# Kernel optimization log

Hardware: AMD Instinct MI355X
Metric: run time of the kernel (lower is better)

Reference implementation:

```python
import jax, jax.numpy as jnp
import numpy as np

B, S, H, IN, OUT = 1024, 512, 512, 2, 2


def setup_inputs() -> dict:
    key = jax.random.key(0)
    ks = jax.random.split(key, 10)
    s = 1.0 / np.sqrt(H)  # torch default uniform init scale for GRU/Linear
    u = lambda k, shp: jax.random.uniform(k, shp, jnp.float32, -s, s)
    return {
        "X0": jax.random.normal(ks[0], (B, OUT), jnp.float32),
        "V": jax.random.normal(ks[1], (B, S, IN), jnp.float32),
        "W_ih": u(ks[2], (3 * H, IN + OUT)),
        "W_hh": u(ks[3], (3 * H, H)),
        "b_ih": u(ks[4], (3 * H,)),
        "b_hh": u(ks[5], (3 * H,)),
        "W1": u(ks[6], (H // 2, H)),
        "b1": u(ks[7], (H // 2,)),
        "W2": u(ks[8], (OUT, H // 2)),
        "b2": u(ks[9], (OUT,)),
    }


def reference(X0, V, W_ih, W_hh, b_ih, b_hh, W1, b1, W2, b2):
    out_size = W2.shape[0]
    hidden = W_hh.shape[1]

    def step(carry, v_t):
        x_prev, h_prev = carry  # [B,out], [B,H]
        linear_pred = x_prev + v_t[:, :out_size]
        gru_in = jnp.concatenate([v_t, x_prev], axis=-1)  # [B, in+out]
        gi = gru_in @ W_ih.T + b_ih  # [B, 3H]
        gh = h_prev @ W_hh.T + b_hh  # [B, 3H]
        i_r, i_z, i_n = jnp.split(gi, 3, axis=-1)
        h_r, h_z, h_n = jnp.split(gh, 3, axis=-1)
        r = jax.nn.sigmoid(i_r + h_r)
        z = jax.nn.sigmoid(i_z + h_z)
        n = jnp.tanh(i_n + r * h_n)
        h_t = (1.0 - z) * n + z * h_prev  # torch GRU cell update
        residual = jax.nn.relu(h_t @ W1.T + b1) @ W2.T + b2
        x_t = linear_pred + residual
        return (x_t, h_t), x_t

    h0 = jnp.zeros((X0.shape[0], hidden), X0.dtype)
    _, xs = jax.lax.scan(step, (X0, h0), jnp.swapaxes(V, 0, 1))  # xs: [S,B,out]
    return jnp.swapaxes(xs, 0, 1)  # [B,S,out]
```

## Files before the change

### kernel.cpp

```cpp
#include <hip/hip_runtime.h>

#define Ssz 512
#define BT  64
#define SLC 32

typedef __attribute__((ext_vector_type(8))) short short8;
typedef __attribute__((ext_vector_type(4))) float f32x4;
typedef __attribute__((ext_vector_type(4))) unsigned uint4v;

#define WS_PW   0u
#define WS_PW1  1572864u
#define WS_HB   1835008u
#define WS_PX   3932160u
#define WS_BAR  4456448u

__device__ __forceinline__ unsigned short f2bf(float f) {
  unsigned int u = __builtin_bit_cast(unsigned int, f);
  u += 0x7fffu + ((u >> 16) & 1u);
  return (unsigned short)(u >> 16);
}
__device__ __forceinline__ float sigm(float x) {
  x = fminf(fmaxf(x, -30.f), 30.f);
  return 1.f / (1.f + __expf(-x));
}
__device__ __forceinline__ float tanh_f(float x) {
  x = fminf(fmaxf(x, -15.f), 15.f);
  float e = __expf(2.f * x);
  return (e - 1.f) / (e + 1.f);
}

__device__ __forceinline__ uint4v gload16(const void* p) {
  uint4v d;
  asm volatile("global_load_dwordx4 %0, %1, off sc0 sc1" : "=v"(d) : "v"(p));
  return d;
}
__device__ __forceinline__ void gstore16(void* p, uint4v v) {
  asm volatile("global_store_dwordx4 %0, %1, off sc0 sc1" :: "v"(p), "v"(v) : "memory");
}
__device__ __forceinline__ void gstore4(void* p, unsigned v) {
  asm volatile("global_store_dword %0, %1, off sc0 sc1" :: "v"(p), "v"(v) : "memory");
}
__device__ __forceinline__ void vwait0() {
  asm volatile("s_waitcnt vmcnt(0)" ::: "memory");
  __builtin_amdgcn_sched_barrier(0);
}

__global__ void pack_whh_k(const float* __restrict__ Wp, unsigned short* __restrict__ dst,
                           unsigned* __restrict__ barz) {
  if (blockIdx.x == 0) {
    for (int i = threadIdx.x; i < 1024; i += 256) barz[i] = 0u;
  }
  int T = blockIdx.x * 256 + threadIdx.x;
  int l  = T & 63;
  int r1 = T >> 6;
  int kk = r1 & 15;
  int r2 = r1 >> 4;
  int q  = r2 % 6;
  int sl = r2 / 6;
  int g = q >> 1, ch = q & 1;
  int j  = g * 512 + sl * 32 + ch * 16 + (l & 15);
  int kb = kk * 32 + (l >> 4) * 8;
  const float* src = Wp + j * 512 + kb;
  short8 o;
#pragma unroll
  for (int e = 0; e < 8; ++e) o[e] = (short)f2bf(src[e]);
  *reinterpret_cast<short8*>(dst + (size_t)T * 8) = o;
}

__global__ void pack_w1_k(const float* __restrict__ W1, unsigned short* __restrict__ dst) {
  int T = blockIdx.x * 256 + threadIdx.x;
  int l  = T & 63;
  int r1 = T >> 6;
  int kk = r1 & 15;
  int sl = r1 >> 4;
  int j  = sl * 16 + (l & 15);
  int kb = kk * 32 + (l >> 4) * 8;
  const float* src = W1 + j * 512 + kb;
  short8 o;
#pragma unroll
  for (int e = 0; e < 8; ++e) o[e] = (short)f2bf(src[e]);
  *reinterpret_cast<short8*>(dst + (size_t)T * 8) = o;
}

__device__ __forceinline__ int haddr(int rowbase, int sw, int ld, int kk) {
  return rowbase + (((ld << 4) + (kk << 6)) ^ sw);
}

__global__ __launch_bounds__(256, 1) void gru_main(
    const float* __restrict__ X0, const float* __restrict__ V,
    const float* __restrict__ Wih, const float* __restrict__ bih,
    const float* __restrict__ bhh, const float* __restrict__ b1,
    const float* __restrict__ W2, const float* __restrict__ b2,
    const unsigned short* __restrict__ PW, const unsigned short* __restrict__ PW1,
    unsigned short* __restrict__ Hb, float* __restrict__ px,
    unsigned* __restrict__ bar, float* __restrict__ out)
{
  __shared__ alignas(16) unsigned short hfull[BT * 512];
  __shared__ alignas(16) unsigned short hstage[BT][40];
  __shared__ alignas(16) float xg[BT][4];

  const int tid = threadIdx.x;
  const int l  = tid & 63, w = tid >> 6;
  const int lm = l & 15,  ld = l >> 4;
  const int rt = blockIdx.x & 15, sl = blockIdx.x >> 4;
  const int rfh = w >> 1, ch = w & 1;
  const int row0 = rt * BT;
  char* hfullB = reinterpret_cast<char*>(hfull);

  unsigned* fl1 = bar + rt * 32;
  unsigned* fl2 = fl1 + 16;

  short8 BW[3][16];
  {
    const char* pwb = reinterpret_cast<const char*>(PW);
#pragma unroll
    for (int g = 0; g < 3; ++g)
#pragma unroll
      for (int kk = 0; kk < 16; ++kk)
        BW[g][kk] = *reinterpret_cast<const short8*>(
            pwb + (size_t)((((sl * 6 + g * 2 + ch) * 16 + kk) * 64 + l) * 16));
  }
  short8 BM[16];
  {
    const char* pw1b = reinterpret_cast<const char*>(PW1);
#pragma unroll
    for (int kk = 0; kk < 16; ++kk)
      BM[kk] = *reinterpret_cast<const short8*>(
          pw1b + (size_t)(((sl * 16 + kk) * 64 + l) * 16));
  }

  const int jcol = sl * SLC + ch * 16 + lm;
  f32x4 wvx[3]; float bi[3], bh[3];
#pragma unroll
  for (int g = 0; g < 3; ++g) {
    int jg = g * 512 + jcol;
    wvx[g] = *reinterpret_cast<const f32x4*>(Wih + (size_t)jg * 4);
    bi[g] = bih[jg];
    bh[g] = bhh[jg];
  }
  const int ic = sl * 16 + lm;
  const float b1v = b1[ic];
  const float w2a = W2[ic], w2b = W2[256 + ic];
  const float b2c = b2[tid & 1];

  float xcur = 0.f;
  if (tid < BT * 2) {
    int row = tid >> 1, c = tid & 1;
    float x0 = X0[(row0 + row) * 2 + c];
    xcur = x0;
    xg[row][2 + c] = x0;
    xg[row][c] = V[(size_t)(row0 + row) * (Ssz * 2) + c];
  }
  float hp[2][4];
#pragma unroll
  for (int q = 0; q < 2; ++q)
#pragma unroll
    for (int r = 0; r < 4; ++r) hp[q][r] = 0.f;
  __syncthreads();

  const int rbA0 = (rfh * 32 + lm) * 1024,      swA0 = ((rfh * 32 + lm) & 7) << 4;
  const int rbA1 = (rfh * 32 + 16 + lm) * 1024, swA1 = ((rfh * 32 + 16 + lm) & 7) << 4;
  const int rbB  = (w * 16 + lm) * 1024,        swB  = ((w * 16 + lm) & 7) << 4;

  for (int i = 0; i <= Ssz; ++i) {
    f32x4 acc[2][3];
#pragma unroll
    for (int q = 0; q < 2; ++q)
#pragma unroll
      for (int g = 0; g < 3; ++g) acc[q][g] = (f32x4){0.f, 0.f, 0.f, 0.f};

    if (i > 0) {
      if (tid == 0) {
        for (;;) {
          uint4v x0 = gload16(fl1 + 0),  x1 = gload16(fl1 + 4);
          uint4v x2 = gload16(fl1 + 8),  x3 = gload16(fl1 + 12);
          vwait0();
          unsigned mn = x0[0];
#pragma unroll
          for (int s = 1; s < 4; ++s) mn = min(mn, x0[s]);
#pragma unroll
          for (int s = 0; s < 4; ++s) { mn = min(mn, x1[s]); mn = min(mn, x2[s]); mn = min(mn, x3[s]); }
          if (mn >= (unsigned)i) break;
          __builtin_amdgcn_s_sleep(2);
        }
      }
      __syncthreads();

      {
        const unsigned short* hsrc = Hb + (size_t)((i - 1) & 1) * (1024 * 512)
                                        + (size_t)row0 * 512;
        uint4v fb[16];
#pragma unroll
        for (int j = 0; j < 16; ++j)
          fb[j] = gload16(hsrc + (size_t)(tid + 256 * j) * 8);
        vwait0();
#pragma unroll
        for (int j = 0; j < 16; ++j) {
          int c = tid + 256 * j;
          int row = c >> 6, c16 = c & 63;
          *reinterpret_cast<uint4v*>(hfullB + row * 1024 + ((c16 * 16) ^ ((row & 7) << 4))) = fb[j];
        }
      }
      __syncthreads();

      {
        f32x4 am = (f32x4){0.f, 0.f, 0.f, 0.f};
#pragma unroll
        for (int kk = 0; kk < 16; ++kk) {
          short8 a = *reinterpret_cast<const short8*>(hfullB + haddr(rbB, swB, ld, kk));
          am = __builtin_amdgcn_mfma_f32_16x16x32_bf16(a, BM[kk], am, 0, 0, 0);
        }
        float pa[4], pb[4];
#pragma unroll
        for (int r = 0; r < 4; ++r) {
          float mv = fmaxf(am[r] + b1v, 0.f);
          pa[r] = mv * w2a;
          pb[r] = mv * w2b;
        }
#pragma unroll
        for (int off = 1; off < 16; off <<= 1)
#pragma unroll
          for (int r = 0; r < 4; ++r) {
            pa[r] += __shfl_xor(pa[r], off);
            pb[r] += __shfl_xor(pb[r], off);
          }
        if (lm == 0) {
#pragma unroll
          for (int r = 0; r < 4; ++r) {
            int row = w * 16 + ld * 4 + r;
            float* p0 = px + ((size_t)(rt * 64 + row) * 2 + 0) * 16 + sl;
            float* p1 = px + ((size_t)(rt * 64 + row) * 2 + 1) * 16 + sl;
            gstore4(p0, __builtin_bit_cast(unsigned, pa[r]));
            gstore4(p1, __builtin_bit_cast(unsigned, pb[r]));
          }
        }
      }
      asm volatile("s_waitcnt vmcnt(0)" ::: "memory");
      __syncthreads();
      if (tid == 0) gstore4(fl2 + sl, (unsigned)i);

#pragma unroll
      for (int kk = 0; kk < 16; ++kk) {
        short8 a0 = *reinterpret_cast<const short8*>(hfullB + haddr(rbA0, swA0, ld, kk));
        short8 a1 = *reinterpret_cast<const short8*>(hfullB + haddr(rbA1, swA1, ld, kk));
        acc[0][0] = __builtin_amdgcn_mfma_f32_16x16x32_bf16(a0, BW[0][kk], acc[0][0], 0, 0, 0);
        acc[1][0] = __builtin_amdgcn_mfma_f32_16x16x32_bf16(a1, BW[0][kk], acc[1][0], 0, 0, 0);
        acc[0][1] = __builtin_amdgcn_mfma_f32_16x16x32_bf16(a0, BW[1][kk], acc[0][1], 0, 0, 0);
        acc[1][1] = __builtin_amdgcn_mfma_f32_16x16x32_bf16(a1, BW[1][kk], acc[1][1], 0, 0, 0);
        acc[0][2] = __builtin_amdgcn_mfma_f32_16x16x32_bf16(a0, BW[2][kk], acc[0][2], 0, 0, 0);
        acc[1][2] = __builtin_amdgcn_mfma_f32_16x16x32_bf16(a1, BW[2][kk], acc[1][2], 0, 0, 0);
      }

      if (tid == 0) {
        for (;;) {
          uint4v x0 = gload16(fl2 + 0),  x1 = gload16(fl2 + 4);
          uint4v x2 = gload16(fl2 + 8),  x3 = gload16(fl2 + 12);
          vwait0();
          unsigned mn = x0[0];
#pragma unroll
          for (int s = 1; s < 4; ++s) mn = min(mn, x0[s]);
#pragma unroll
          for (int s = 0; s < 4; ++s) { mn = min(mn, x1[s]); mn = min(mn, x2[s]); mn = min(mn, x3[s]); }
          if (mn >= (unsigned)i) break;
          __builtin_amdgcn_s_sleep(2);
        }
      }
      __syncthreads();

      if (tid < BT * 2) {
        int row = tid >> 1, c = tid & 1;
        const float* pc = px + ((size_t)(rt * 64 + row) * 2 + c) * 16;
        f32x4 s0 = __builtin_bit_cast(f32x4, gload16(pc + 0));
        f32x4 s1 = __builtin_bit_cast(f32x4, gload16(pc + 4));
        f32x4 s2 = __builtin_bit_cast(f32x4, gload16(pc + 8));
        f32x4 s3 = __builtin_bit_cast(f32x4, gload16(pc + 12));
        vwait0();
        float s = b2c;
#pragma unroll
        for (int r = 0; r < 4; ++r) s += s0[r] + s1[r] + s2[r] + s3[r];
        float vprev = xg[row][c];
        float xt = xcur + vprev + s;
        xcur = xt;
        if (sl == 0) out[(size_t)(row0 + row) * (Ssz * 2) + (i - 1) * 2 + c] = xt;
        xg[row][2 + c] = xt;
        xg[row][c] = (i < Ssz) ? V[(size_t)(row0 + row) * (Ssz * 2) + i * 2 + c] : 0.f;
      }
      __syncthreads();
    }

    if (i < Ssz) {
#pragma unroll
      for (int rf2 = 0; rf2 < 2; ++rf2) {
#pragma unroll
        for (int r = 0; r < 4; ++r) {
          const int m = rfh * 32 + rf2 * 16 + ld * 4 + r;
          const f32x4 xv = *reinterpret_cast<const f32x4*>(&xg[m][0]);
          float gv0 = wvx[0][0]*xv[0] + wvx[0][1]*xv[1] + wvx[0][2]*xv[2] + wvx[0][3]*xv[3];
          float gv1 = wvx[1][0]*xv[0] + wvx[1][1]*xv[1] + wvx[1][2]*xv[2] + wvx[1][3]*xv[3];
          float gv2 = wvx[2][0]*xv[0] + wvx[2][1]*xv[1] + wvx[2][2]*xv[2] + wvx[2][3]*xv[3];
          float rr = sigm(gv0 + bi[0] + bh[0] + acc[rf2][0][r]);
          float zz = sigm(gv1 + bi[1] + bh[1] + acc[rf2][1][r]);
          float nn = tanh_f(gv2 + bi[2] + rr * (acc[rf2][2][r] + bh[2]));
          float ht = (1.f - zz) * nn + zz * hp[rf2][r];
          hp[rf2][r] = ht;
          hstage[m][ch * 16 + lm] = f2bf(ht);
        }
      }
      __syncthreads();

      {
        int row = tid >> 2, seg = tid & 3;
        uint4v hv = *reinterpret_cast<const uint4v*>(&hstage[row][seg * 8]);
        gstore16(Hb + (size_t)(i & 1) * (1024 * 512)
                    + (size_t)(row0 + row) * 512 + sl * SLC + seg * 8, hv);
      }
      asm volatile("s_waitcnt vmcnt(0)" ::: "memory");
      __syncthreads();
      if (tid == 0) gstore4(fl1 + sl, (unsigned)(i + 1));
    }
  }
}

extern "C" void kernel_launch(void* const* d_in, const int* in_sizes, int n_in,
                              void* d_out, int out_size, void* d_ws, size_t ws_size,
                              hipStream_t stream) {
  const float* X0  = (const float*)d_in[0];
  const float* V   = (const float*)d_in[1];
  const float* Wih = (const float*)d_in[2];
  const float* Whh = (const float*)d_in[3];
  const float* bih = (const float*)d_in[4];
  const float* bhh = (const float*)d_in[5];
  const float* W1  = (const float*)d_in[6];
  const float* b1  = (const float*)d_in[7];
  const float* W2  = (const float*)d_in[8];
  const float* b2  = (const float*)d_in[9];
  float* out = (float*)d_out;

  char* ws = (char*)d_ws;
  unsigned short* PW  = (unsigned short*)(ws + WS_PW);
  unsigned short* PW1 = (unsigned short*)(ws + WS_PW1);
  unsigned short* Hb  = (unsigned short*)(ws + WS_HB);
  float*          px  = (float*)(ws + WS_PX);
  unsigned*       bar = (unsigned*)(ws + WS_BAR);

  pack_whh_k<<<384, 256, 0, stream>>>(Whh, PW, bar);
  pack_w1_k<<<64, 256, 0, stream>>>(W1, PW1);
  gru_main<<<256, 256, 0, stream>>>(X0, V, Wih, bih, bhh, b1, W2, b2,
                                    PW, PW1, Hb, px, bar, out);
}
```

Measured before the change: 3.967 ms.

## Poll flags per-wave and drop block barriers around hidden-state gather

```diff
diff --git a/kernel.cpp b/kernel.cpp
--- a/kernel.cpp
+++ b/kernel.cpp
@@ -6,7 +6,9 @@
 
 typedef __attribute__((ext_vector_type(8))) short short8;
 typedef __attribute__((ext_vector_type(4))) float f32x4;
+typedef __attribute__((ext_vector_type(2))) float f32x2;
 typedef __attribute__((ext_vector_type(4))) unsigned uint4v;
+typedef __attribute__((ext_vector_type(2))) unsigned uint2v;
 
 #define WS_PW   0u
 #define WS_PW1  1572864u
@@ -32,6 +34,11 @@
 __device__ __forceinline__ uint4v gload16(const void* p) {
   uint4v d;
   asm volatile("global_load_dwordx4 %0, %1, off sc0 sc1" : "=v"(d) : "v"(p));
+  return d;
+}
+__device__ __forceinline__ unsigned gload4(const void* p) {
+  unsigned d;
+  asm volatile("global_load_dword %0, %1, off sc0 sc1" : "=v"(d) : "v"(p));
   return d;
 }
 __device__ __forceinline__ void gstore16(void* p, uint4v v) {
@@ -170,38 +177,30 @@
       for (int g = 0; g < 3; ++g) acc[q][g] = (f32x4){0.f, 0.f, 0.f, 0.f};
 
     if (i > 0) {
-      if (tid == 0) {
+      {
+        const unsigned* fp = fl1 + (l & 15);
         for (;;) {
-          uint4v x0 = gload16(fl1 + 0),  x1 = gload16(fl1 + 4);
-          uint4v x2 = gload16(fl1 + 8),  x3 = gload16(fl1 + 12);
+          unsigned v = gload4(fp);
           vwait0();
-          unsigned mn = x0[0];
-#pragma unroll
-          for (int s = 1; s < 4; ++s) mn = min(mn, x0[s]);
-#pragma unroll
-          for (int s = 0; s < 4; ++s) { mn = min(mn, x1[s]); mn = min(mn, x2[s]); mn = min(mn, x3[s]); }
-          if (mn >= (unsigned)i) break;
-          __builtin_amdgcn_s_sleep(2);
-        }
-      }
-      __syncthreads();
+          if (__all((int)(v >= (unsigned)i))) break;
+          __builtin_amdgcn_s_sleep(1);
+        }
+      }
 
       {
-        const unsigned short* hsrc = Hb + (size_t)((i - 1) & 1) * (1024 * 512)
-                                        + (size_t)row0 * 512;
+        const char* hsrc = reinterpret_cast<const char*>(
+            Hb + (size_t)((i - 1) & 1) * (1024 * 512) + (size_t)row0 * 512);
         uint4v fb[16];
 #pragma unroll
         for (int j = 0; j < 16; ++j)
-          fb[j] = gload16(hsrc + (size_t)(tid + 256 * j) * 8);
+          fb[j] = gload16(hsrc + (size_t)(w * 16 + j) * 1024 + l * 16);
         vwait0();
 #pragma unroll
         for (int j = 0; j < 16; ++j) {
-          int c = tid + 256 * j;
-          int row = c >> 6, c16 = c & 63;
-          *reinterpret_cast<uint4v*>(hfullB + row * 1024 + ((c16 * 16) ^ ((row & 7) << 4))) = fb[j];
-        }
-      }
-      __syncthreads();
+          const int m = w * 16 + j;
+          *reinterpret_cast<uint4v*>(hfullB + m * 1024 + ((l * 16) ^ ((m & 7) << 4))) = fb[j];
+        }
+      }
 
       {
         f32x4 am = (f32x4){0.f, 0.f, 0.f, 0.f};
@@ -239,34 +238,29 @@
       __syncthreads();
       if (tid == 0) gstore4(fl2 + sl, (unsigned)i);
 
-#pragma unroll
-      for (int kk = 0; kk < 16; ++kk) {
-        short8 a0 = *reinterpret_cast<const short8*>(hfullB + haddr(rbA0, swA0, ld, kk));
-        short8 a1 = *reinterpret_cast<const short8*>(hfullB + haddr(rbA1, swA1, ld, kk));
-        acc[0][0] = __builtin_amdgcn_mfma_f32_16x16x32_bf16(a0, BW[0][kk], acc[0][0], 0, 0, 0);
-        acc[1][0] = __builtin_amdgcn_mfma_f32_16x16x32_bf16(a1, BW[0][kk], acc[1][0], 0, 0, 0);
-        acc[0][1] = __builtin_amdgcn_mfma_f32_16x16x32_bf16(a0, BW[1][kk], acc[0][1], 0, 0, 0);
-        acc[1][1] = __builtin_amdgcn_mfma_f32_16x16x32_bf16(a1, BW[1][kk], acc[1][1], 0, 0, 0);
-        acc[0][2] = __builtin_amdgcn_mfma_f32_16x16x32_bf16(a0, BW[2][kk], acc[0][2], 0, 0, 0);
-        acc[1][2] = __builtin_amdgcn_mfma_f32_16x16x32_bf16(a1, BW[2][kk], acc[1][2], 0, 0, 0);
-      }
-
-      if (tid == 0) {
+      if (i < Ssz) {
+#pragma unroll
+        for (int kk = 0; kk < 16; ++kk) {
+          short8 a0 = *reinterpret_cast<const short8*>(hfullB + haddr(rbA0, swA0, ld, kk));
+          short8 a1 = *reinterpret_cast<const short8*>(hfullB + haddr(rbA1, swA1, ld, kk));
+          acc[0][0] = __builtin_amdgcn_mfma_f32_16x16x32_bf16(a0, BW[0][kk], acc[0][0], 0, 0, 0);
+          acc[1][0] = __builtin_amdgcn_mfma_f32_16x16x32_bf16(a1, BW[0][kk], acc[1][0], 0, 0, 0);
+          acc[0][1] = __builtin_amdgcn_mfma_f32_16x16x32_bf16(a0, BW[1][kk], acc[0][1], 0, 0, 0);
+          acc[1][1] = __builtin_amdgcn_mfma_f32_16x16x32_bf16(a1, BW[1][kk], acc[1][1], 0, 0, 0);
+          acc[0][2] = __builtin_amdgcn_mfma_f32_16x16x32_bf16(a0, BW[2][kk], acc[0][2], 0, 0, 0);
+          acc[1][2] = __builtin_amdgcn_mfma_f32_16x16x32_bf16(a1, BW[2][kk], acc[1][2], 0, 0, 0);
+        }
+      }
+
+      if (w < 2) {
+        const unsigned* fp = fl2 + (l & 15);
         for (;;) {
-          uint4v x0 = gload16(fl2 + 0),  x1 = gload16(fl2 + 4);
-          uint4v x2 = gload16(fl2 + 8),  x3 = gload16(fl2 + 12);
+          unsigned v = gload4(fp);
           vwait0();
-          unsigned mn = x0[0];
-#pragma unroll
-          for (int s = 1; s < 4; ++s) mn = min(mn, x0[s]);
-#pragma unroll
-          for (int s = 0; s < 4; ++s) { mn = min(mn, x1[s]); mn = min(mn, x2[s]); mn = min(mn, x3[s]); }
-          if (mn >= (unsigned)i) break;
-          __builtin_amdgcn_s_sleep(2);
-        }
-      }
-      __syncthreads();
-
+          if (__all((int)(v >= (unsigned)i))) break;
+          __builtin_amdgcn_s_sleep(1);
+        }
+      }
       if (tid < BT * 2) {
         int row = tid >> 1, c = tid & 1;
         const float* pc = px + ((size_t)(rt * 64 + row) * 2 + c) * 16;
```

New measurement: 3.931 ms. About the same (-0.9%).
